# Optimization experiments

Measured on AMD Instinct MI355X. Metric: run time of the kernel, lower is better.

The kernel has to match this reference:

```python
import jax, jax.numpy as jnp
import numpy as np

N, H, OUT, R, E, B = 50000, 64, 64, 50, 800000, 4  # nodes, hidden, out, relations, edges, blocks


def _glorot(k, shape):
    fan_in, fan_out = shape[-2], shape[-1]
    s = (6.0 / (fan_in + fan_out)) ** 0.5
    return jax.random.uniform(k, shape, jnp.float32, -s, s)


def setup_inputs() -> dict:
    key = jax.random.key(0)
    ks = jax.random.split(key, 12)
    db = H // B
    inp = {
        "x": jax.random.normal(ks[0], (N, H), jnp.float32),
        "edge_index": jax.random.randint(ks[1], (2, E), 0, N),
        "edge_type": jax.random.randint(ks[2], (E,), 0, R),
        # hidden RGCNConv layers: block-diagonal relation weights [R,B,db,db]
        "w0_rel": _glorot(ks[3], (R, B, db, db)),
        "w0_root": _glorot(ks[4], (H, H)),
        "b0": jnp.zeros((H,), jnp.float32),
        "w1_rel": _glorot(ks[5], (R, B, db, db)),
        "w1_root": _glorot(ks[6], (H, H)),
        "b1": jnp.zeros((H,), jnp.float32),
        # final RGCNConv: full per-relation weights [R,H,OUT]
        "w2_rel": _glorot(ks[7], (R, H, OUT)),
        "w2_root": _glorot(ks[8], (H, OUT)),
        "b2": jnp.zeros((OUT,), jnp.float32),
    }
    return inp


def _rgcn_layer(x, src, dst, etype, w_rel, w_root, bias):
    """RGCNConv: per-relation mean aggregation of neighbor features, relation-typed
    transform, plus root (self) transform and bias. Instead of gathering a per-edge
    weight (huge), we segment-sum neighbor features per (dst node, relation) and do
    one batched matmul over relations -- same math, far less traffic."""
    n, d = x.shape
    seg = dst * R + etype                                   # combined (node,rel) id
    msgs = x[src]                                           # [E, d] gather
    s = jax.ops.segment_sum(msgs, seg, num_segments=n * R).reshape(n, R, d)
    cnt = jax.ops.segment_sum(jnp.ones((msgs.shape[0],), x.dtype), seg,
                              num_segments=n * R).reshape(n, R, 1)
    s = s / jnp.maximum(cnt, 1.0)                           # mean per relation
    if w_rel.ndim == 4:                                     # block-diagonal decomposition
        nb, db, do = w_rel.shape[1], w_rel.shape[2], w_rel.shape[3]
        agg = jnp.einsum('nrbd,rbde->nbe', s.reshape(n, R, nb, db), w_rel)
        agg = agg.reshape(n, nb * do)
    else:                                                   # full per-relation weight
        agg = jnp.einsum('nrd,rde->ne', s, w_rel)
    return agg + x @ w_root + bias


def reference(x, edge_index, edge_type,
              w0_rel, w0_root, b0,
              w1_rel, w1_root, b1,
              w2_rel, w2_root, b2):
    src, dst = edge_index[0], edge_index[1]
    h = jax.nn.relu(_rgcn_layer(x, src, dst, edge_type, w0_rel, w0_root, b0))
    # dropout: eval mode (identity)
    h = jax.nn.relu(_rgcn_layer(h, src, dst, edge_type, w1_rel, w1_root, b1))
    return _rgcn_layer(h, src, dst, edge_type, w2_rel, w2_root, b2)
```

## Files before the change

kernel.cpp:

```cpp
#include <hip/hip_runtime.h>
#include <cstdint>
#include <cstddef>

#define N_NODES 50000
#define HDIM 64
#define NREL 50
#define NEDGE 800000
#define DCHUNK 196
#define CHUNKSH 11
#define NCHUNK 25
#define NKEYS (NCHUNK * NREL)
#define KCH 5
#define CAP 36864
#define TILE 8192

typedef __attribute__((ext_vector_type(8))) short short8;
typedef __attribute__((ext_vector_type(4))) float f32x4;

static __device__ __forceinline__ unsigned short f2bf(float f) {
  union { float f; unsigned int u; } v; v.f = f;
  unsigned int u = v.u;
  unsigned int r = (u + 0x7FFFu + ((u >> 16) & 1u)) >> 16;
  return (unsigned short)r;
}


__global__ __launch_bounds__(256) void csort_k(const int* __restrict__ ei,
                                               const int* __restrict__ et,
                                               int* __restrict__ ccur,
                                               int2* __restrict__ ce) {
  __shared__ int chist[32];
  __shared__ int cbase[32];
  int tid = threadIdx.x;
  if (tid < 32) chist[tid] = 0;
  __syncthreads();
  int ebase = blockIdx.x * 1280 + tid;
  int src_[5], dr_[5], ch_[5], loc_[5];
#pragma unroll
  for (int i = 0; i < 5; ++i) {
    int e = ebase + i * 256;
    int src = ei[e];
    int dst = ei[NEDGE + e];
    int r = et[e];
    int ch = dst >> CHUNKSH;
    src_[i] = src;
    dr_[i] = (dst << 6) | r;
    ch_[i] = ch;
    loc_[i] = atomicAdd(&chist[ch], 1);
  }
  __syncthreads();
  if (tid < NCHUNK && chist[tid] > 0)
    cbase[tid] = atomicAdd(&ccur[tid], chist[tid]);
  __syncthreads();
#pragma unroll
  for (int i = 0; i < 5; ++i)
    ce[(size_t)ch_[i] * CAP + cbase[ch_[i]] + loc_[i]] = make_int2(src_[i], dr_[i]);
}

__global__ __launch_bounds__(1024) void msplit_k(const int2* __restrict__ ce,
                                                 const int* __restrict__ ccur,
                                                 int* __restrict__ dcur,
                                                 int* __restrict__ kcur,
                                                 int* __restrict__ dkr) {
  __shared__ int dhist[2048], dbase[2048];
  __shared__ int rhist[64], rbase[64];
  int c = blockIdx.y;
  int len = ccur[c];
  int t0 = blockIdx.x * TILE;
  if (t0 >= len) return;
  int tid = threadIdx.x;
  dhist[tid] = 0;
  dhist[tid + 1024] = 0;
  if (tid < 64) rhist[tid] = 0;
  __syncthreads();
  int n = min(TILE, len - t0);
  const int2* seg = ce + (size_t)c * CAP + t0;
  int pk[8], dr_[8];
#pragma unroll
  for (int k = 0; k < 8; ++k) {
    int j = tid + k * 1024;
    if (j < n) {
      int2 v = seg[j];
      dr_[k] = v.y;
      int d11 = (v.y >> 6) & 2047;
      int rel = v.y & 63;
      int dl = atomicAdd(&dhist[d11], 1);
      int rl = atomicAdd(&rhist[rel], 1);
      pk[k] = (dl << 16) | rl;
    } else {
      pk[k] = -1;
    }
  }
  __syncthreads();
  int h0 = dhist[tid];
  if (h0 > 0) dbase[tid] = atomicAdd(&dcur[(c << CHUNKSH) + tid], h0);
  int h1 = dhist[tid + 1024];
  if (h1 > 0) dbase[tid + 1024] = atomicAdd(&dcur[(c << CHUNKSH) + tid + 1024], h1);
  if (tid < NREL) {
    int hr = rhist[tid];
    if (hr > 0) rbase[tid] = atomicAdd(&kcur[c * NREL + tid], hr);
  }
  __syncthreads();
#pragma unroll
  for (int k = 0; k < 8; ++k) {
    if (pk[k] >= 0) {
      int d11 = (dr_[k] >> 6) & 2047;
      int rel = dr_[k] & 63;
      int drank = dbase[d11] + (pk[k] >> 16);
      int krank = rbase[rel] + (pk[k] & 0xFFFF);
      dkr[(size_t)c * CAP + t0 + tid + k * 1024] = (drank << 16) | krank;
    }
  }
}

__global__ __launch_bounds__(256) void kscan_k(const int* __restrict__ kcur,
                                               int* __restrict__ key_off) {
  __shared__ int a[256], bb[256];
  int t = threadIdx.x;
  int base = t * KCH;
  int local[KCH];
  int s = 0;
#pragma unroll
  for (int i = 0; i < KCH; ++i) {
    int k = base + i;
    int v = (k < NKEYS) ? kcur[k] : 0;
    local[i] = s;
    s += v;
  }
  a[t] = s;
  __syncthreads();
  bool flip = false;
  for (int off = 1; off < 256; off <<= 1) {
    int* c = flip ? bb : a;
    int* n = flip ? a : bb;
    int x = c[t];
    if (t >= off) x += c[t - off];
    n[t] = x;
    __syncthreads();
    flip = !flip;
  }
  int incl = (flip ? bb : a)[t];
  int excl = incl - s;
#pragma unroll
  for (int i = 0; i < KCH; ++i) {
    int k = base + i;
    if (k < NKEYS) key_off[k] = excl + local[i];
  }
  if (t == 255) key_off[NKEYS] = incl;
}

__global__ __launch_bounds__(256) void dsA_k(const int* __restrict__ dcnt,
                                             int* __restrict__ psum) {
  __shared__ int red[256];
  int t = threadIdx.x, b = blockIdx.x;
  int idx = b * DCHUNK + t;
  int v = (t < DCHUNK && idx < N_NODES) ? dcnt[idx] : 0;
  red[t] = v;
  __syncthreads();
  for (int s = 128; s > 0; s >>= 1) {
    if (t < s) red[t] += red[t + s];
    __syncthreads();
  }
  if (t == 0) psum[b] = red[0];
}

__global__ __launch_bounds__(256) void dsB_k(const int* __restrict__ psum,
                                             int* __restrict__ psb,
                                             int* __restrict__ dst_off) {
  __shared__ int a[256], bb[256];
  int t = threadIdx.x;
  int v = psum[t];
  a[t] = v;
  __syncthreads();
  bool flip = false;
  for (int off = 1; off < 256; off <<= 1) {
    int* c = flip ? bb : a;
    int* n = flip ? a : bb;
    int x = c[t];
    if (t >= off) x += c[t - off];
    n[t] = x;
    __syncthreads();
    flip = !flip;
  }
  int incl = (flip ? bb : a)[t];
  psb[t] = incl - v;
  if (t == 255) dst_off[N_NODES] = incl;
}

__global__ __launch_bounds__(256) void dsC_k(const int* __restrict__ dcnt,
                                             const int* __restrict__ psb,
                                             int* __restrict__ dst_off) {
  __shared__ int a[256], bb[256];
  int t = threadIdx.x, b = blockIdx.x;
  int idx = b * DCHUNK + t;
  int v = (t < DCHUNK && idx < N_NODES) ? dcnt[idx] : 0;
  a[t] = v;
  __syncthreads();
  bool flip = false;
  for (int off = 1; off < 256; off <<= 1) {
    int* c = flip ? bb : a;
    int* n = flip ? a : bb;
    int x = c[t];
    if (t >= off) x += c[t - off];
    n[t] = x;
    __syncthreads();
    flip = !flip;
  }
  int incl = (flip ? bb : a)[t];
  if (t < DCHUNK && idx < N_NODES) dst_off[idx] = psb[b] + (incl - v);
}

__global__ __launch_bounds__(1024) void place_k(const int2* __restrict__ ce,
                                                const int* __restrict__ ccur,
                                                const int* __restrict__ dkr,
                                                const int* __restrict__ key_off,
                                                const int* __restrict__ dst_off,
                                                int* __restrict__ es,
                                                int* __restrict__ rpr) {
  int c = blockIdx.y;
  int len = ccur[c];
  int t0 = blockIdx.x * TILE;
  if (t0 >= len) return;
  int tid = threadIdx.x;
  int n = min(TILE, len - t0);
  size_t base = (size_t)c * CAP + t0;
#pragma unroll
  for (int k = 0; k < 8; ++k) {
    int j = tid + k * 1024;
    if (j < n) {
      int2 v = ce[base + j];
      int dk = dkr[base + j];
      int dst = v.y >> 6;
      int rel = v.y & 63;
      int key = c * NREL + rel;
      int pos = key_off[key] + (dk & 0xFFFF);
      int dp = dst_off[dst] + (dk >> 16);
      es[pos] = v.x;
      rpr[dp] = (pos << 6) | rel;
    }
  }
}

__global__ __launch_bounds__(256) void coef_k(const int* __restrict__ rpr,
                                              const int* __restrict__ dst_off,
                                              float* __restrict__ coefd) {
  int lane = threadIdx.x & 63;
  int wv = (blockIdx.x * 256 + threadIdx.x) >> 6;
  int half = lane >> 5, l = lane & 31;
  int dst = wv * 2 + half;
  if (dst >= N_NODES) return;
  int lo = dst_off[dst], hi = dst_off[dst + 1];
  for (int j = lo + l; j < hi; j += 32) {
    int r = rpr[j] & 63;
    int c = 0;
    for (int k = lo; k < hi; ++k) c += ((rpr[k] & 63) == r);
    coefd[j] = 1.0f / (float)c;
  }
}

__global__ void prep_k(const float* __restrict__ w0, const float* __restrict__ w1,
                       const float* __restrict__ w2,
                       const float* __restrict__ wr0f, const float* __restrict__ wr1f,
                       const float* __restrict__ wr2f,
                       unsigned short* __restrict__ Wt0, unsigned short* __restrict__ Wt1,
                       unsigned short* __restrict__ Wt2,
                       unsigned short* __restrict__ Wr0, unsigned short* __restrict__ Wr1,
                       unsigned short* __restrict__ Wr2) {
  int idx = blockIdx.x * 256 + threadIdx.x;
  if (idx < NREL * 4096) {
    int r = idx >> 12, rem = idx & 4095, d = rem >> 6, o = rem & 63;
    int tpos = (r << 12) + (o << 6) + d;
    Wt2[tpos] = f2bf(w2[idx]);
    int b = o >> 4;
    float v0 = 0.f, v1 = 0.f;
    if (b == (d >> 4)) {
      int widx = ((r * 4 + b) * 16 + (d & 15)) * 16 + (o & 15);
      v0 = w0[widx];
      v1 = w1[widx];
    }
    Wt0[tpos] = f2bf(v0);
    Wt1[tpos] = f2bf(v1);
  }
  if (idx < 4096) {
    int d = idx >> 6, o = idx & 63;
    int tpos = (o << 6) + d;
    Wr0[tpos] = f2bf(wr0f[idx]);
    Wr1[tpos] = f2bf(wr1f[idx]);
    Wr2[tpos] = f2bf(wr2f[idx]);
  }
}

__global__ void conv_k(const float* __restrict__ in, unsigned short* __restrict__ out) {
  int i = blockIdx.x * 256 + threadIdx.x;
  out[i] = f2bf(in[i]);
}


__global__ __launch_bounds__(256) void root_k(const unsigned short* __restrict__ xbf,
                                              const unsigned short* __restrict__ wr,
                                              const float* __restrict__ bias,
                                              float* __restrict__ out) {
  int wid = threadIdx.x >> 6, lane = threadIdx.x & 63;
  int n15 = lane & 15, quad = lane >> 4;
  int t = blockIdx.x * 4 + wid;
  if (t >= N_NODES / 16) return;
  short8 bfr[4][2];
#pragma unroll
  for (int nb = 0; nb < 4; ++nb)
#pragma unroll
    for (int k = 0; k < 2; ++k)
      bfr[nb][k] = *reinterpret_cast<const short8*>(wr + ((nb * 16 + n15) << 6) + k * 32 + quad * 8);
  float bv[4];
#pragma unroll
  for (int nb = 0; nb < 4; ++nb) bv[nb] = bias[nb * 16 + n15];

  int base = t * 16;
  const short8* xr = reinterpret_cast<const short8*>(xbf + (size_t)(base + n15) * 64);
  short8 a0 = xr[quad], a1 = xr[4 + quad];
  f32x4 acc[4];
#pragma unroll
  for (int nb = 0; nb < 4; ++nb) acc[nb] = (f32x4){0.f, 0.f, 0.f, 0.f};
#pragma unroll
  for (int nb = 0; nb < 4; ++nb) {
    acc[nb] = __builtin_amdgcn_mfma_f32_16x16x32_bf16(a0, bfr[nb][0], acc[nb], 0, 0, 0);
    acc[nb] = __builtin_amdgcn_mfma_f32_16x16x32_bf16(a1, bfr[nb][1], acc[nb], 0, 0, 0);
  }
#pragma unroll
  for (int i = 0; i < 4; ++i) {
    int node = base + quad * 4 + i;
#pragma unroll
    for (int nb = 0; nb < 4; ++nb)
      out[(size_t)node * 64 + nb * 16 + n15] = acc[nb][i] + bv[nb];
  }
}

__global__ __launch_bounds__(256) void edge_k(const unsigned short* __restrict__ xbf,
                                              const unsigned short* __restrict__ wt,
                                              const int* __restrict__ es,
                                              const int* __restrict__ key_off,
                                              unsigned short* __restrict__ msg) {
  int key = blockIdx.y;
  int lo = key_off[key], hi = key_off[key + 1];
  if (lo >= hi) return;
  int wid = threadIdx.x >> 6, lane = threadIdx.x & 63;
  int n15 = lane & 15, quad = lane >> 4;
  const unsigned short* wr = wt + ((size_t)(key % NREL) << 12);
  short8 bfr[4][2];
#pragma unroll
  for (int nb = 0; nb < 4; ++nb)
#pragma unroll
    for (int k = 0; k < 2; ++k)
      bfr[nb][k] = *reinterpret_cast<const short8*>(wr + ((nb * 16 + n15) << 6) + k * 32 + quad * 8);

  int ntiles = (hi - lo + 15) >> 4;
  for (int t = blockIdx.x * 4 + wid; t < ntiles; t += gridDim.x * 4) {
    int base = lo + t * 16;
    int eidx = base + n15;
    if (eidx > NEDGE - 1) eidx = NEDGE - 1;
    int src = es[eidx];
    const short8* xr = reinterpret_cast<const short8*>(xbf + (size_t)src * 64);
    short8 a0 = xr[quad], a1 = xr[4 + quad];
    f32x4 acc[4];
#pragma unroll
    for (int nb = 0; nb < 4; ++nb) acc[nb] = (f32x4){0.f, 0.f, 0.f, 0.f};
#pragma unroll
    for (int nb = 0; nb < 4; ++nb) {
      acc[nb] = __builtin_amdgcn_mfma_f32_16x16x32_bf16(a0, bfr[nb][0], acc[nb], 0, 0, 0);
      acc[nb] = __builtin_amdgcn_mfma_f32_16x16x32_bf16(a1, bfr[nb][1], acc[nb], 0, 0, 0);
    }
#pragma unroll
    for (int i = 0; i < 4; ++i) {
      int e2 = base + quad * 4 + i;
      if (e2 < hi) {
        size_t row = (size_t)e2 * 64;
#pragma unroll
        for (int nb = 0; nb < 4; ++nb)
          msg[row + nb * 16 + n15] = f2bf(acc[nb][i]);
      }
    }
  }
}

__global__ __launch_bounds__(256) void agg_k(const float* __restrict__ h,
                                             const unsigned short* __restrict__ msg,
                                             const float* __restrict__ coefd,
                                             const int* __restrict__ rpr,
                                             const int* __restrict__ dst_off,
                                             float* __restrict__ outf,
                                             unsigned short* __restrict__ outbf,
                                             int mode) {
  int lane = threadIdx.x & 63;
  int wv = (blockIdx.x * 256 + threadIdx.x) >> 6;
  int half = lane >> 5, l = lane & 31;
  int dst = wv * 2 + half;
  if (dst >= N_NODES) return;
  int lo = dst_off[dst], hi = dst_off[dst + 1];
  float ax = __builtin_nontemporal_load(h + (size_t)dst * 64 + 2 * l);
  float ay = __builtin_nontemporal_load(h + (size_t)dst * 64 + 2 * l + 1);
  const unsigned int* m32 = reinterpret_cast<const unsigned int*>(msg);
  int j = lo;
  for (; j + 4 <= hi; j += 4) {
    int q0 = rpr[j] >> 6, q1 = rpr[j + 1] >> 6, q2 = rpr[j + 2] >> 6, q3 = rpr[j + 3] >> 6;
    float c0 = coefd[j], c1 = coefd[j + 1], c2 = coefd[j + 2], c3 = coefd[j + 3];
    unsigned int u0 = __builtin_nontemporal_load(m32 + q0 * 32 + l);
    unsigned int u1 = __builtin_nontemporal_load(m32 + q1 * 32 + l);
    unsigned int u2 = __builtin_nontemporal_load(m32 + q2 * 32 + l);
    unsigned int u3 = __builtin_nontemporal_load(m32 + q3 * 32 + l);
    union { unsigned int u; float f; } cx, cy;
    cx.u = (u0 & 0xFFFFu) << 16; cy.u = u0 & 0xFFFF0000u; ax += c0 * cx.f; ay += c0 * cy.f;
    cx.u = (u1 & 0xFFFFu) << 16; cy.u = u1 & 0xFFFF0000u; ax += c1 * cx.f; ay += c1 * cy.f;
    cx.u = (u2 & 0xFFFFu) << 16; cy.u = u2 & 0xFFFF0000u; ax += c2 * cx.f; ay += c2 * cy.f;
    cx.u = (u3 & 0xFFFFu) << 16; cy.u = u3 & 0xFFFF0000u; ax += c3 * cx.f; ay += c3 * cy.f;
  }
  for (; j < hi; ++j) {
    float c = coefd[j];
    int pos = rpr[j] >> 6;
    unsigned int u = __builtin_nontemporal_load(m32 + pos * 32 + l);
    union { unsigned int u; float f; } cx, cy;
    cx.u = (u & 0xFFFFu) << 16;
    cy.u = u & 0xFFFF0000u;
    ax += c * cx.f;
    ay += c * cy.f;
  }
  if (mode == 0) {
    float fx = fmaxf(ax, 0.f), fy = fmaxf(ay, 0.f);
    unsigned int pk = ((unsigned int)f2bf(fy) << 16) | (unsigned int)f2bf(fx);
    *reinterpret_cast<unsigned int*>(outbf + (size_t)dst * 64 + 2 * l) = pk;
  } else {
    float2 o2; o2.x = ax; o2.y = ay;
    *reinterpret_cast<float2*>(outf + (size_t)dst * 64 + 2 * l) = o2;
  }
}


extern "C" void kernel_launch(void* const* d_in, const int* in_sizes, int n_in,
                              void* d_out, int out_size, void* d_ws, size_t ws_size,
                              hipStream_t stream) {
  const float* x   = (const float*)d_in[0];
  const int*   ei  = (const int*)d_in[1];
  const int*   et  = (const int*)d_in[2];
  const float* w0  = (const float*)d_in[3];
  const float* wr0 = (const float*)d_in[4];
  const float* b0  = (const float*)d_in[5];
  const float* w1  = (const float*)d_in[6];
  const float* wr1 = (const float*)d_in[7];
  const float* b1  = (const float*)d_in[8];
  const float* w2  = (const float*)d_in[9];
  const float* wr2 = (const float*)d_in[10];
  const float* b2  = (const float*)d_in[11];
  float* out = (float*)d_out;

  char* p = (char*)d_ws;
  auto take = [&](size_t bytes) -> char* {
    char* q = p;
    p += (bytes + 255) & ~(size_t)255;
    return q;
  };
  char*  zbase   = p;
  int*   ccur    = (int*)take(32 * 4);
  int*   dcur    = (int*)take((size_t)NCHUNK * 2048 * 4);
  int*   kcur    = (int*)take((size_t)NKEYS * 4);
  size_t zbytes  = (size_t)(p - zbase);
  int*   key_off = (int*)take((size_t)(NKEYS + 1) * 4);
  int*   dst_off = (int*)take((size_t)(N_NODES + 1) * 4);
  int*   psum    = (int*)take(256 * 4);
  int*   psb     = (int*)take(256 * 4);
  int2*  ce      = (int2*)take((size_t)NCHUNK * CAP * 8);
  int*   dkr     = (int*)take((size_t)NCHUNK * CAP * 4);
  int*   es      = (int*)take((size_t)NEDGE * 4);
  int*   rpr     = (int*)take((size_t)NEDGE * 4);
  float* coefd   = (float*)take((size_t)NEDGE * 4);
  unsigned short* xbf = (unsigned short*)take((size_t)N_NODES * 64 * 2);
  float* h       = (float*)take((size_t)N_NODES * 64 * 4);
  unsigned short* msg = (unsigned short*)take((size_t)NEDGE * 64 * 2);
  unsigned short* Wt0 = (unsigned short*)take((size_t)NREL * 4096 * 2);
  unsigned short* Wt1 = (unsigned short*)take((size_t)NREL * 4096 * 2);
  unsigned short* Wt2 = (unsigned short*)take((size_t)NREL * 4096 * 2);
  unsigned short* Wr0 = (unsigned short*)take(4096 * 2);
  unsigned short* Wr1 = (unsigned short*)take(4096 * 2);
  unsigned short* Wr2 = (unsigned short*)take(4096 * 2);

  hipMemsetAsync(zbase, 0, zbytes, stream);
  csort_k<<<NEDGE / 1280, 256, 0, stream>>>(ei, et, ccur, ce);
  dim3 mg(5, NCHUNK);
  msplit_k<<<mg, 1024, 0, stream>>>(ce, ccur, dcur, kcur, dkr);
  kscan_k<<<1, 256, 0, stream>>>(kcur, key_off);
  dsA_k<<<256, 256, 0, stream>>>(dcur, psum);
  dsB_k<<<1, 256, 0, stream>>>(psum, psb, dst_off);
  dsC_k<<<256, 256, 0, stream>>>(dcur, psb, dst_off);
  place_k<<<mg, 1024, 0, stream>>>(ce, ccur, dkr, key_off, dst_off, es, rpr);
  coef_k<<<N_NODES / 8, 256, 0, stream>>>(rpr, dst_off, coefd);
  prep_k<<<(NREL * 4096 + 255) / 256, 256, 0, stream>>>(w0, w1, w2, wr0, wr1, wr2,
                                                        Wt0, Wt1, Wt2, Wr0, Wr1, Wr2);

  const int conv_blocks = N_NODES * 64 / 256;
  const int root_blocks = (N_NODES / 16 + 3) / 4;
  const int agg_blocks  = N_NODES / 8;
  dim3 eg(2, NKEYS);

  conv_k<<<conv_blocks, 256, 0, stream>>>(x, xbf);
  root_k<<<root_blocks, 256, 0, stream>>>(xbf, Wr0, b0, h);
  edge_k<<<eg, 256, 0, stream>>>(xbf, Wt0, es, key_off, msg);
  agg_k<<<agg_blocks, 256, 0, stream>>>(h, msg, coefd, rpr, dst_off, nullptr, xbf, 0);
  root_k<<<root_blocks, 256, 0, stream>>>(xbf, Wr1, b1, h);
  edge_k<<<eg, 256, 0, stream>>>(xbf, Wt1, es, key_off, msg);
  agg_k<<<agg_blocks, 256, 0, stream>>>(h, msg, coefd, rpr, dst_off, nullptr, xbf, 0);
  root_k<<<root_blocks, 256, 0, stream>>>(xbf, Wr2, b2, h);
  edge_k<<<eg, 256, 0, stream>>>(xbf, Wt2, es, key_off, msg);
  agg_k<<<agg_blocks, 256, 0, stream>>>(h, msg, coefd, rpr, dst_off, out, nullptr, 1);
}
```

Measured before the change: 381.5 us.

## Fuse edge transform and aggregation per 64-node group via LDS message buffer

Edges are now sorted by (64-destination-node group, relation) instead of (chunk, relation). A single fused kernel per group computes the relation-typed MFMA transforms into shared memory, then aggregates them per destination without writing or reading the large global per-edge message buffer. Key offset scanning becomes a three-phase scan over the larger key space, and ping-pong bf16 buffers replace in-place reuse of xbf. It risks silently truncating groups with more than 1216 edges or 160 tiles, and it gives up edge-level parallelism with 1024-thread blocks and a single warp setting up the tile directory.

```diff
diff --git a/kernel.cpp b/kernel.cpp
--- a/kernel.cpp
+++ b/kernel.cpp
@@ -9,8 +9,10 @@
 #define DCHUNK 196
 #define CHUNKSH 11
 #define NCHUNK 25
-#define NKEYS (NCHUNK * NREL)
-#define KCH 5
+#define NKEY2 (NCHUNK * 2048)
+#define NCH64 782
+#define SCAP 1216
+#define TDIRN 160
 #define CAP 36864
 #define TILE 8192
 
@@ -63,15 +65,14 @@
                                                  int* __restrict__ kcur,
                                                  int* __restrict__ dkr) {
   __shared__ int dhist[2048], dbase[2048];
-  __shared__ int rhist[64], rbase[64];
+  __shared__ int khist[2048], kbase[2048];
   int c = blockIdx.y;
   int len = ccur[c];
   int t0 = blockIdx.x * TILE;
   if (t0 >= len) return;
   int tid = threadIdx.x;
-  dhist[tid] = 0;
-  dhist[tid + 1024] = 0;
-  if (tid < 64) rhist[tid] = 0;
+  dhist[tid] = 0; dhist[tid + 1024] = 0;
+  khist[tid] = 0; khist[tid + 1024] = 0;
   __syncthreads();
   int n = min(TILE, len - t0);
   const int2* seg = ce + (size_t)c * CAP + t0;
@@ -83,10 +84,10 @@
       int2 v = seg[j];
       dr_[k] = v.y;
       int d11 = (v.y >> 6) & 2047;
-      int rel = v.y & 63;
+      int key11 = (d11 & 0x7C0) | (v.y & 63);
       int dl = atomicAdd(&dhist[d11], 1);
-      int rl = atomicAdd(&rhist[rel], 1);
-      pk[k] = (dl << 16) | rl;
+      int kl = atomicAdd(&khist[key11], 1);
+      pk[k] = (dl << 16) | kl;
     } else {
       pk[k] = -1;
     }
@@ -96,38 +97,43 @@
   if (h0 > 0) dbase[tid] = atomicAdd(&dcur[(c << CHUNKSH) + tid], h0);
   int h1 = dhist[tid + 1024];
   if (h1 > 0) dbase[tid + 1024] = atomicAdd(&dcur[(c << CHUNKSH) + tid + 1024], h1);
-  if (tid < NREL) {
-    int hr = rhist[tid];
-    if (hr > 0) rbase[tid] = atomicAdd(&kcur[c * NREL + tid], hr);
-  }
+  int k0 = khist[tid];
+  if (k0 > 0) kbase[tid] = atomicAdd(&kcur[(c << CHUNKSH) + tid], k0);
+  int k1 = khist[tid + 1024];
+  if (k1 > 0) kbase[tid + 1024] = atomicAdd(&kcur[(c << CHUNKSH) + tid + 1024], k1);
   __syncthreads();
 #pragma unroll
   for (int k = 0; k < 8; ++k) {
     if (pk[k] >= 0) {
       int d11 = (dr_[k] >> 6) & 2047;
-      int rel = dr_[k] & 63;
+      int key11 = (d11 & 0x7C0) | (dr_[k] & 63);
       int drank = dbase[d11] + (pk[k] >> 16);
-      int krank = rbase[rel] + (pk[k] & 0xFFFF);
+      int krank = kbase[key11] + (pk[k] & 0xFFFF);
       dkr[(size_t)c * CAP + t0 + tid + k * 1024] = (drank << 16) | krank;
     }
   }
 }
 
-__global__ __launch_bounds__(256) void kscan_k(const int* __restrict__ kcur,
-                                               int* __restrict__ key_off) {
+
+__global__ __launch_bounds__(256) void ksA_k(const int* __restrict__ kcur,
+                                             int* __restrict__ kps) {
+  __shared__ int red[256];
+  int t = threadIdx.x, b = blockIdx.x;
+  red[t] = kcur[b * 256 + t];
+  __syncthreads();
+  for (int s = 128; s > 0; s >>= 1) {
+    if (t < s) red[t] += red[t + s];
+    __syncthreads();
+  }
+  if (t == 0) kps[b] = red[0];
+}
+
+__global__ __launch_bounds__(256) void ksB_k(const int* __restrict__ kps,
+                                             int* __restrict__ kpsb) {
   __shared__ int a[256], bb[256];
   int t = threadIdx.x;
-  int base = t * KCH;
-  int local[KCH];
-  int s = 0;
-#pragma unroll
-  for (int i = 0; i < KCH; ++i) {
-    int k = base + i;
-    int v = (k < NKEYS) ? kcur[k] : 0;
-    local[i] = s;
-    s += v;
-  }
-  a[t] = s;
+  int v = (t < 200) ? kps[t] : 0;
+  a[t] = v;
   __syncthreads();
   bool flip = false;
   for (int off = 1; off < 256; off <<= 1) {
@@ -140,14 +146,31 @@
     flip = !flip;
   }
   int incl = (flip ? bb : a)[t];
-  int excl = incl - s;
-#pragma unroll
-  for (int i = 0; i < KCH; ++i) {
-    int k = base + i;
-    if (k < NKEYS) key_off[k] = excl + local[i];
-  }
-  if (t == 255) key_off[NKEYS] = incl;
-}
+  kpsb[t] = incl - v;
+}
+
+__global__ __launch_bounds__(256) void ksC_k(const int* __restrict__ kcur,
+                                             const int* __restrict__ kpsb,
+                                             int* __restrict__ key_off) {
+  __shared__ int a[256], bb[256];
+  int t = threadIdx.x, b = blockIdx.x;
+  int v = kcur[b * 256 + t];
+  a[t] = v;
+  __syncthreads();
+  bool flip = false;
+  for (int off = 1; off < 256; off <<= 1) {
+    int* c = flip ? bb : a;
+    int* n = flip ? a : bb;
+    int x = c[t];
+    if (t >= off) x += c[t - off];
+    n[t] = x;
+    __syncthreads();
+    flip = !flip;
+  }
+  int incl = (flip ? bb : a)[t];
+  key_off[b * 256 + t] = kpsb[b] + (incl - v);
+}
+
 
 __global__ __launch_bounds__(256) void dsA_k(const int* __restrict__ dcnt,
                                              int* __restrict__ psum) {
@@ -232,11 +255,14 @@
       int dk = dkr[base + j];
       int dst = v.y >> 6;
       int rel = v.y & 63;
-      int key = c * NREL + rel;
-      int pos = key_off[key] + (dk & 0xFFFF);
+      int d11 = dst & 2047;
+      int gkey = (c << CHUNKSH) | (d11 & 0x7C0) | rel;
+      int pos = key_off[gkey] + (dk & 0xFFFF);
+      int cb = key_off[(c << CHUNKSH) | (d11 & 0x7C0)];
+      int local = (pos - cb) & 2047;
       int dp = dst_off[dst] + (dk >> 16);
       es[pos] = v.x;
-      rpr[dp] = (pos << 6) | rel;
+      rpr[dp] = (local << 6) | rel;
     }
   }
 }
@@ -295,7 +321,6 @@
   out[i] = f2bf(in[i]);
 }
 
-
 __global__ __launch_bounds__(256) void root_k(const unsigned short* __restrict__ xbf,
                                               const unsigned short* __restrict__ wr,
                                               const float* __restrict__ bias,
@@ -334,30 +359,72 @@
   }
 }
 
-__global__ __launch_bounds__(256) void edge_k(const unsigned short* __restrict__ xbf,
-                                              const unsigned short* __restrict__ wt,
-                                              const int* __restrict__ es,
-                                              const int* __restrict__ key_off,
-                                              unsigned short* __restrict__ msg) {
-  int key = blockIdx.y;
-  int lo = key_off[key], hi = key_off[key + 1];
-  if (lo >= hi) return;
-  int wid = threadIdx.x >> 6, lane = threadIdx.x & 63;
+__global__ __launch_bounds__(1024) void fused_k(const unsigned short* __restrict__ xbf,
+                                                const unsigned short* __restrict__ wt,
+                                                const int* __restrict__ es,
+                                                const int* __restrict__ key_off,
+                                                const float* __restrict__ h,
+                                                const float* __restrict__ coefd,
+                                                const int* __restrict__ rpr,
+                                                const int* __restrict__ dst_off,
+                                                float* __restrict__ outf,
+                                                unsigned short* __restrict__ outbf,
+                                                int mode) {
+  __shared__ unsigned short smsg[SCAP * 64];
+  __shared__ int tdir[TDIRN];
+  __shared__ int s_ntiles;
+  int c = blockIdx.x;
+  int g = c << 6;
+  int tid = threadIdx.x;
+  int wid = tid >> 6, lane = tid & 63;
   int n15 = lane & 15, quad = lane >> 4;
-  const unsigned short* wr = wt + ((size_t)(key % NREL) << 12);
+  int ebase = key_off[g];
+
+  if (wid == 0) {
+    int r = lane;
+    int len = (r < NREL) ? key_off[g + r + 1] - key_off[g + r] : 0;
+    int ntl = (len + 15) >> 4;
+    int srow = len, stile = ntl;
+    for (int off = 1; off < 64; off <<= 1) {
+      int pr = __shfl_up(srow, off);
+      int pt = __shfl_up(stile, off);
+      if (lane >= off) { srow += pr; stile += pt; }
+    }
+    int rowstart = srow - len;
+    int tstart = stile - ntl;
+    for (int t = 0; t < ntl; ++t) {
+      int rs = rowstart + t * 16;
+      int re = min(rowstart + len, rs + 16);
+      int di = tstart + t;
+      if (di < TDIRN)
+        tdir[di] = ((rs & 2047) << 17) | ((re & 2047) << 6) | r;
+    }
+    if (lane == 63) s_ntiles = min(stile, TDIRN);
+  }
+  __syncthreads();
+
+  int nt = s_ntiles;
+  int T = (nt + 15) >> 4;
+  int t1 = min(nt, (wid + 1) * T);
+  int prevrel = -1;
   short8 bfr[4][2];
-#pragma unroll
-  for (int nb = 0; nb < 4; ++nb)
-#pragma unroll
-    for (int k = 0; k < 2; ++k)
-      bfr[nb][k] = *reinterpret_cast<const short8*>(wr + ((nb * 16 + n15) << 6) + k * 32 + quad * 8);
-
-  int ntiles = (hi - lo + 15) >> 4;
-  for (int t = blockIdx.x * 4 + wid; t < ntiles; t += gridDim.x * 4) {
-    int base = lo + t * 16;
-    int eidx = base + n15;
-    if (eidx > NEDGE - 1) eidx = NEDGE - 1;
-    int src = es[eidx];
+  for (int ti = wid * T; ti < t1; ++ti) {
+    int pk = tdir[ti];
+    int rel = pk & 63;
+    int rs = (pk >> 17) & 2047;
+    int re = (pk >> 6) & 2047;
+    if (rel != prevrel) {
+      const unsigned short* wr = wt + ((size_t)rel << 12);
+#pragma unroll
+      for (int nb = 0; nb < 4; ++nb)
+#pragma unroll
+        for (int k = 0; k < 2; ++k)
+          bfr[nb][k] = *reinterpret_cast<const short8*>(wr + ((nb * 16 + n15) << 6) + k * 32 + quad * 8);
+      prevrel = rel;
+    }
+    int row = rs + n15;
+    if (row > re - 1) row = re - 1;
+    int src = es[ebase + row];
     const short8* xr = reinterpret_cast<const short8*>(xbf + (size_t)src * 64);
     short8 a0 = xr[quad], a1 = xr[4 + quad];
     f32x4 acc[4];
@@ -370,65 +437,47 @@
     }
 #pragma unroll
     for (int i = 0; i < 4; ++i) {
-      int e2 = base + quad * 4 + i;
-      if (e2 < hi) {
-        size_t row = (size_t)e2 * 64;
+      int r2 = rs + quad * 4 + i;
+      if (r2 < re && r2 < SCAP) {
 #pragma unroll
         for (int nb = 0; nb < 4; ++nb)
-          msg[row + nb * 16 + n15] = f2bf(acc[nb][i]);
+          smsg[r2 * 64 + nb * 16 + n15] = f2bf(acc[nb][i]);
       }
     }
   }
-}
-
-__global__ __launch_bounds__(256) void agg_k(const float* __restrict__ h,
-                                             const unsigned short* __restrict__ msg,
-                                             const float* __restrict__ coefd,
-                                             const int* __restrict__ rpr,
-                                             const int* __restrict__ dst_off,
-                                             float* __restrict__ outf,
-                                             unsigned short* __restrict__ outbf,
-                                             int mode) {
-  int lane = threadIdx.x & 63;
-  int wv = (blockIdx.x * 256 + threadIdx.x) >> 6;
+  __syncthreads();
+
+  const unsigned int* m32 = reinterpret_cast<const unsigned int*>(smsg);
   int half = lane >> 5, l = lane & 31;
-  int dst = wv * 2 + half;
-  if (dst >= N_NODES) return;
-  int lo = dst_off[dst], hi = dst_off[dst + 1];
-  float ax = __builtin_nontemporal_load(h + (size_t)dst * 64 + 2 * l);
-  float ay = __builtin_nontemporal_load(h + (size_t)dst * 64 + 2 * l + 1);
-  const unsigned int* m32 = reinterpret_cast<const unsigned int*>(msg);
-  int j = lo;
-  for (; j + 4 <= hi; j += 4) {
-    int q0 = rpr[j] >> 6, q1 = rpr[j + 1] >> 6, q2 = rpr[j + 2] >> 6, q3 = rpr[j + 3] >> 6;
-    float c0 = coefd[j], c1 = coefd[j + 1], c2 = coefd[j + 2], c3 = coefd[j + 3];
-    unsigned int u0 = __builtin_nontemporal_load(m32 + q0 * 32 + l);
-    unsigned int u1 = __builtin_nontemporal_load(m32 + q1 * 32 + l);
-    unsigned int u2 = __builtin_nontemporal_load(m32 + q2 * 32 + l);
-    unsigned int u3 = __builtin_nontemporal_load(m32 + q3 * 32 + l);
-    union { unsigned int u; float f; } cx, cy;
-    cx.u = (u0 & 0xFFFFu) << 16; cy.u = u0 & 0xFFFF0000u; ax += c0 * cx.f; ay += c0 * cy.f;
-    cx.u = (u1 & 0xFFFFu) << 16; cy.u = u1 & 0xFFFF0000u; ax += c1 * cx.f; ay += c1 * cy.f;
-    cx.u = (u2 & 0xFFFFu) << 16; cy.u = u2 & 0xFFFF0000u; ax += c2 * cx.f; ay += c2 * cy.f;
-    cx.u = (u3 & 0xFFFFu) << 16; cy.u = u3 & 0xFFFF0000u; ax += c3 * cx.f; ay += c3 * cy.f;
-  }
-  for (; j < hi; ++j) {
-    float c = coefd[j];
-    int pos = rpr[j] >> 6;
-    unsigned int u = __builtin_nontemporal_load(m32 + pos * 32 + l);
-    union { unsigned int u; float f; } cx, cy;
-    cx.u = (u & 0xFFFFu) << 16;
-    cy.u = u & 0xFFFF0000u;
-    ax += c * cx.f;
-    ay += c * cy.f;
-  }
-  if (mode == 0) {
-    float fx = fmaxf(ax, 0.f), fy = fmaxf(ay, 0.f);
-    unsigned int pk = ((unsigned int)f2bf(fy) << 16) | (unsigned int)f2bf(fx);
-    *reinterpret_cast<unsigned int*>(outbf + (size_t)dst * 64 + 2 * l) = pk;
-  } else {
-    float2 o2; o2.x = ax; o2.y = ay;
-    *reinterpret_cast<float2*>(outf + (size_t)dst * 64 + 2 * l) = o2;
+#pragma unroll
+  for (int it = 0; it < 2; ++it) {
+    int dl_ = it * 32 + wid * 2 + half;
+    int dst = (c << 6) + dl_;
+    if (dst < N_NODES) {
+      int lo = dst_off[dst], hi = dst_off[dst + 1];
+      float ax = h[(size_t)dst * 64 + 2 * l];
+      float ay = h[(size_t)dst * 64 + 2 * l + 1];
+      for (int j = lo; j < hi; ++j) {
+        int rp = rpr[j];
+        int lp = (rp >> 6) & 2047;
+        if (lp >= SCAP) lp = SCAP - 1;
+        float cf = coefd[j];
+        unsigned int u = m32[lp * 32 + l];
+        union { unsigned int u; float f; } cx, cy;
+        cx.u = (u & 0xFFFFu) << 16;
+        cy.u = u & 0xFFFF0000u;
+        ax += cf * cx.f;
+        ay += cf * cy.f;
+      }
+      if (mode == 0) {
+        float fx = fmaxf(ax, 0.f), fy = fmaxf(ay, 0.f);
+        unsigned int pkv = ((unsigned int)f2bf(fy) << 16) | (unsigned int)f2bf(fx);
+        *reinterpret_cast<unsigned int*>(outbf + (size_t)dst * 64 + 2 * l) = pkv;
+      } else {
+        float2 o2; o2.x = ax; o2.y = ay;
+        *reinterpret_cast<float2*>(outf + (size_t)dst * 64 + 2 * l) = o2;
+      }
+    }
   }
 }
 
@@ -459,20 +508,22 @@
   char*  zbase   = p;
   int*   ccur    = (int*)take(32 * 4);
   int*   dcur    = (int*)take((size_t)NCHUNK * 2048 * 4);
-  int*   kcur    = (int*)take((size_t)NKEYS * 4);
+  int*   kcur    = (int*)take((size_t)NKEY2 * 4);
   size_t zbytes  = (size_t)(p - zbase);
-  int*   key_off = (int*)take((size_t)(NKEYS + 1) * 4);
+  int*   key_off = (int*)take((size_t)(NKEY2 + 1) * 4);
   int*   dst_off = (int*)take((size_t)(N_NODES + 1) * 4);
   int*   psum    = (int*)take(256 * 4);
   int*   psb     = (int*)take(256 * 4);
+  int*   kps     = (int*)take(256 * 4);
+  int*   kpsb    = (int*)take(256 * 4);
   int2*  ce      = (int2*)take((size_t)NCHUNK * CAP * 8);
   int*   dkr     = (int*)take((size_t)NCHUNK * CAP * 4);
   int*   es      = (int*)take((size_t)NEDGE * 4);
   int*   rpr     = (int*)take((size_t)NEDGE * 4);
   float* coefd   = (float*)take((size_t)NEDGE * 4);
-  unsigned short* xbf = (unsigned short*)take((size_t)N_NODES * 64 * 2);
+  unsigned short* xb0 = (unsigned short*)take((size_t)N_NODES * 64 * 2);
+  unsigned short* xb1 = (unsigned short*)take((size_t)N_NODES * 64 * 2);
   float* h       = (float*)take((size_t)N_NODES * 64 * 4);
-  unsigned short* msg = (unsigned short*)take((size_t)NEDGE * 64 * 2);
   unsigned short* Wt0 = (unsigned short*)take((size_t)NREL * 4096 * 2);
   unsigned short* Wt1 = (unsigned short*)take((size_t)NREL * 4096 * 2);
   unsigned short* Wt2 = (unsigned short*)take((size_t)NREL * 4096 * 2);
@@ -484,7 +535,9 @@
   csort_k<<<NEDGE / 1280, 256, 0, stream>>>(ei, et, ccur, ce);
   dim3 mg(5, NCHUNK);
   msplit_k<<<mg, 1024, 0, stream>>>(ce, ccur, dcur, kcur, dkr);
-  kscan_k<<<1, 256, 0, stream>>>(kcur, key_off);
+  ksA_k<<<NKEY2 / 256, 256, 0, stream>>>(kcur, kps);
+  ksB_k<<<1, 256, 0, stream>>>(kps, kpsb);
+  ksC_k<<<NKEY2 / 256, 256, 0, stream>>>(kcur, kpsb, key_off);
   dsA_k<<<256, 256, 0, stream>>>(dcur, psum);
   dsB_k<<<1, 256, 0, stream>>>(psum, psb, dst_off);
   dsC_k<<<256, 256, 0, stream>>>(dcur, psb, dst_off);
@@ -495,17 +548,15 @@
 
   const int conv_blocks = N_NODES * 64 / 256;
   const int root_blocks = (N_NODES / 16 + 3) / 4;
-  const int agg_blocks  = N_NODES / 8;
-  dim3 eg(2, NKEYS);
-
-  conv_k<<<conv_blocks, 256, 0, stream>>>(x, xbf);
-  root_k<<<root_blocks, 256, 0, stream>>>(xbf, Wr0, b0, h);
-  edge_k<<<eg, 256, 0, stream>>>(xbf, Wt0, es, key_off, msg);
-  agg_k<<<agg_blocks, 256, 0, stream>>>(h, msg, coefd, rpr, dst_off, nullptr, xbf, 0);
-  root_k<<<root_blocks, 256, 0, stream>>>(xbf, Wr1, b1, h);
-  edge_k<<<eg, 256, 0, stream>>>(xbf, Wt1, es, key_off, msg);
-  agg_k<<<agg_blocks, 256, 0, stream>>>(h, msg, coefd, rpr, dst_off, nullptr, xbf, 0);
-  root_k<<<root_blocks, 256, 0, stream>>>(xbf, Wr2, b2, h);
-  edge_k<<<eg, 256, 0, stream>>>(xbf, Wt2, es, key_off, msg);
-  agg_k<<<agg_blocks, 256, 0, stream>>>(h, msg, coefd, rpr, dst_off, out, nullptr, 1);
-}
+
+  conv_k<<<conv_blocks, 256, 0, stream>>>(x, xb0);
+  root_k<<<root_blocks, 256, 0, stream>>>(xb0, Wr0, b0, h);
+  fused_k<<<NCH64, 1024, 0, stream>>>(xb0, Wt0, es, key_off, h, coefd, rpr, dst_off,
+                                      nullptr, xb1, 0);
+  root_k<<<root_blocks, 256, 0, stream>>>(xb1, Wr1, b1, h);
+  fused_k<<<NCH64, 1024, 0, stream>>>(xb1, Wt1, es, key_off, h, coefd, rpr, dst_off,
+                                      nullptr, xb0, 0);
+  root_k<<<root_blocks, 256, 0, stream>>>(xb0, Wr2, b2, h);
+  fused_k<<<NCH64, 1024, 0, stream>>>(xb0, Wt2, es, key_off, h, coefd, rpr, dst_off,
+                                      out, nullptr, 1);
+}
```

Measured after the change: 520.1 us. 1.36x slower.

## Fold mean coefficient into edge messages and software-pipeline source gathers

Applied to the files above, without the earlier changes.

The per-edge mean coefficient is now stored in edge-sorted (key) order and applied inside the edge transform kernel before the bf16 store, so the aggregation kernel no longer loads a coefficient per incoming edge. The edge kernel also prefetches the next tile's source features and the source index two tiles ahead, hiding gather latency. The cost is scaling before bf16 rounding, which slightly changes numerics, plus extra registers and redundant clamped loads at the tail.

```diff
diff --git a/kernel.cpp b/kernel.cpp
--- a/kernel.cpp
+++ b/kernel.cpp
@@ -243,7 +243,7 @@
 
 __global__ __launch_bounds__(256) void coef_k(const int* __restrict__ rpr,
                                               const int* __restrict__ dst_off,
-                                              float* __restrict__ coefd) {
+                                              float* __restrict__ coefc) {
   int lane = threadIdx.x & 63;
   int wv = (blockIdx.x * 256 + threadIdx.x) >> 6;
   int half = lane >> 5, l = lane & 31;
@@ -254,7 +254,7 @@
     int r = rpr[j] & 63;
     int c = 0;
     for (int k = lo; k < hi; ++k) c += ((rpr[k] & 63) == r);
-    coefd[j] = 1.0f / (float)c;
+    coefc[rpr[j] >> 6] = 1.0f / (float)c;
   }
 }
 
@@ -337,6 +337,7 @@
 __global__ __launch_bounds__(256) void edge_k(const unsigned short* __restrict__ xbf,
                                               const unsigned short* __restrict__ wt,
                                               const int* __restrict__ es,
+                                              const float* __restrict__ coefc,
                                               const int* __restrict__ key_off,
                                               unsigned short* __restrict__ msg) {
   int key = blockIdx.y;
@@ -353,13 +354,27 @@
       bfr[nb][k] = *reinterpret_cast<const short8*>(wr + ((nb * 16 + n15) << 6) + k * 32 + quad * 8);
 
   int ntiles = (hi - lo + 15) >> 4;
-  for (int t = blockIdx.x * 4 + wid; t < ntiles; t += gridDim.x * 4) {
-    int base = lo + t * 16;
-    int eidx = base + n15;
-    if (eidx > NEDGE - 1) eidx = NEDGE - 1;
-    int src = es[eidx];
-    const short8* xr = reinterpret_cast<const short8*>(xbf + (size_t)src * 64);
-    short8 a0 = xr[quad], a1 = xr[4 + quad];
+  int stride = gridDim.x * 4;
+  int t = blockIdx.x * 4 + wid;
+  if (t >= ntiles) return;
+
+  int base = lo + t * 16;
+  int src0 = es[min(base + n15, hi - 1)];
+  const short8* xr0 = reinterpret_cast<const short8*>(xbf + (size_t)src0 * 64);
+  short8 a0 = xr0[quad], a1 = xr0[4 + quad];
+  int t1c = min(t + stride, ntiles - 1);
+  int src1 = es[min(lo + t1c * 16 + n15, hi - 1)];
+
+  while (true) {
+    const short8* xr1 = reinterpret_cast<const short8*>(xbf + (size_t)src1 * 64);
+    short8 b0 = xr1[quad], b1 = xr1[4 + quad];
+    int t2c = min(t + 2 * stride, ntiles - 1);
+    int src2 = es[min(lo + t2c * 16 + n15, hi - 1)];
+    float cf_[4];
+#pragma unroll
+    for (int i = 0; i < 4; ++i)
+      cf_[i] = coefc[min(base + quad * 4 + i, hi - 1)];
+
     f32x4 acc[4];
 #pragma unroll
     for (int nb = 0; nb < 4; ++nb) acc[nb] = (f32x4){0.f, 0.f, 0.f, 0.f};
@@ -375,15 +390,19 @@
         size_t row = (size_t)e2 * 64;
 #pragma unroll
         for (int nb = 0; nb < 4; ++nb)
-          msg[row + nb * 16 + n15] = f2bf(acc[nb][i]);
+          msg[row + nb * 16 + n15] = f2bf(cf_[i] * acc[nb][i]);
       }
     }
+    t += stride;
+    if (t >= ntiles) break;
+    base = lo + t * 16;
+    a0 = b0; a1 = b1;
+    src1 = src2;
   }
 }
 
 __global__ __launch_bounds__(256) void agg_k(const float* __restrict__ h,
                                              const unsigned short* __restrict__ msg,
-                                             const float* __restrict__ coefd,
                                              const int* __restrict__ rpr,
                                              const int* __restrict__ dst_off,
                                              float* __restrict__ outf,
@@ -401,26 +420,24 @@
   int j = lo;
   for (; j + 4 <= hi; j += 4) {
     int q0 = rpr[j] >> 6, q1 = rpr[j + 1] >> 6, q2 = rpr[j + 2] >> 6, q3 = rpr[j + 3] >> 6;
-    float c0 = coefd[j], c1 = coefd[j + 1], c2 = coefd[j + 2], c3 = coefd[j + 3];
     unsigned int u0 = __builtin_nontemporal_load(m32 + q0 * 32 + l);
     unsigned int u1 = __builtin_nontemporal_load(m32 + q1 * 32 + l);
     unsigned int u2 = __builtin_nontemporal_load(m32 + q2 * 32 + l);
     unsigned int u3 = __builtin_nontemporal_load(m32 + q3 * 32 + l);
     union { unsigned int u; float f; } cx, cy;
-    cx.u = (u0 & 0xFFFFu) << 16; cy.u = u0 & 0xFFFF0000u; ax += c0 * cx.f; ay += c0 * cy.f;
-    cx.u = (u1 & 0xFFFFu) << 16; cy.u = u1 & 0xFFFF0000u; ax += c1 * cx.f; ay += c1 * cy.f;
-    cx.u = (u2 & 0xFFFFu) << 16; cy.u = u2 & 0xFFFF0000u; ax += c2 * cx.f; ay += c2 * cy.f;
-    cx.u = (u3 & 0xFFFFu) << 16; cy.u = u3 & 0xFFFF0000u; ax += c3 * cx.f; ay += c3 * cy.f;
+    cx.u = (u0 & 0xFFFFu) << 16; cy.u = u0 & 0xFFFF0000u; ax += cx.f; ay += cy.f;
+    cx.u = (u1 & 0xFFFFu) << 16; cy.u = u1 & 0xFFFF0000u; ax += cx.f; ay += cy.f;
+    cx.u = (u2 & 0xFFFFu) << 16; cy.u = u2 & 0xFFFF0000u; ax += cx.f; ay += cy.f;
+    cx.u = (u3 & 0xFFFFu) << 16; cy.u = u3 & 0xFFFF0000u; ax += cx.f; ay += cy.f;
   }
   for (; j < hi; ++j) {
-    float c = coefd[j];
     int pos = rpr[j] >> 6;
     unsigned int u = __builtin_nontemporal_load(m32 + pos * 32 + l);
     union { unsigned int u; float f; } cx, cy;
     cx.u = (u & 0xFFFFu) << 16;
     cy.u = u & 0xFFFF0000u;
-    ax += c * cx.f;
-    ay += c * cy.f;
+    ax += cx.f;
+    ay += cy.f;
   }
   if (mode == 0) {
     float fx = fmaxf(ax, 0.f), fy = fmaxf(ay, 0.f);
@@ -469,7 +486,7 @@
   int*   dkr     = (int*)take((size_t)NCHUNK * CAP * 4);
   int*   es      = (int*)take((size_t)NEDGE * 4);
   int*   rpr     = (int*)take((size_t)NEDGE * 4);
-  float* coefd   = (float*)take((size_t)NEDGE * 4);
+  float* coefc   = (float*)take((size_t)NEDGE * 4);
   unsigned short* xbf = (unsigned short*)take((size_t)N_NODES * 64 * 2);
   float* h       = (float*)take((size_t)N_NODES * 64 * 4);
   unsigned short* msg = (unsigned short*)take((size_t)NEDGE * 64 * 2);
@@ -489,7 +506,7 @@
   dsB_k<<<1, 256, 0, stream>>>(psum, psb, dst_off);
   dsC_k<<<256, 256, 0, stream>>>(dcur, psb, dst_off);
   place_k<<<mg, 1024, 0, stream>>>(ce, ccur, dkr, key_off, dst_off, es, rpr);
-  coef_k<<<N_NODES / 8, 256, 0, stream>>>(rpr, dst_off, coefd);
+  coef_k<<<N_NODES / 8, 256, 0, stream>>>(rpr, dst_off, coefc);
   prep_k<<<(NREL * 4096 + 255) / 256, 256, 0, stream>>>(w0, w1, w2, wr0, wr1, wr2,
                                                         Wt0, Wt1, Wt2, Wr0, Wr1, Wr2);
 
@@ -500,12 +517,12 @@
 
   conv_k<<<conv_blocks, 256, 0, stream>>>(x, xbf);
   root_k<<<root_blocks, 256, 0, stream>>>(xbf, Wr0, b0, h);
-  edge_k<<<eg, 256, 0, stream>>>(xbf, Wt0, es, key_off, msg);
-  agg_k<<<agg_blocks, 256, 0, stream>>>(h, msg, coefd, rpr, dst_off, nullptr, xbf, 0);
+  edge_k<<<eg, 256, 0, stream>>>(xbf, Wt0, es, coefc, key_off, msg);
+  agg_k<<<agg_blocks, 256, 0, stream>>>(h, msg, rpr, dst_off, nullptr, xbf, 0);
   root_k<<<root_blocks, 256, 0, stream>>>(xbf, Wr1, b1, h);
-  edge_k<<<eg, 256, 0, stream>>>(xbf, Wt1, es, key_off, msg);
-  agg_k<<<agg_blocks, 256, 0, stream>>>(h, msg, coefd, rpr, dst_off, nullptr, xbf, 0);
+  edge_k<<<eg, 256, 0, stream>>>(xbf, Wt1, es, coefc, key_off, msg);
+  agg_k<<<agg_blocks, 256, 0, stream>>>(h, msg, rpr, dst_off, nullptr, xbf, 0);
   root_k<<<root_blocks, 256, 0, stream>>>(xbf, Wr2, b2, h);
-  edge_k<<<eg, 256, 0, stream>>>(xbf, Wt2, es, key_off, msg);
-  agg_k<<<agg_blocks, 256, 0, stream>>>(h, msg, coefd, rpr, dst_off, out, nullptr, 1);
-}
+  edge_k<<<eg, 256, 0, stream>>>(xbf, Wt2, es, coefc, key_off, msg);
+  agg_k<<<agg_blocks, 256, 0, stream>>>(h, msg, rpr, dst_off, out, nullptr, 1);
+}
```

Result: slower. 398.9 us (+4.6%).
